# Kernel tuning notes

Measured on AMD Instinct MI355X. Metric: run time of the kernel, lower is better.

The kernel has to match this reference:

```python
import jax, jax.numpy as jnp
import numpy as np

_A1 = jnp.array([[1.,0.,0.,0.],[0.,1.,0.,0.],[0.,0.,1.,0.],[0.,0.,0.,1.]], dtype=jnp.float32)
_AI = jnp.array([[0.,-1.,0.,0.],[1.,0.,0.,0.],[0.,0.,0.,-1.],[0.,0.,1.,0.]], dtype=jnp.float32)
_AJ = jnp.array([[0.,0.,-1.,0.],[0.,0.,0.,1.],[1.,0.,0.,0.],[0.,-1.,0.,0.]], dtype=jnp.float32)
_AK = jnp.array([[0.,0.,0.,-1.],[0.,0.,-1.,0.],[0.,1.,0.,0.],[1.,0.,0.,0.]], dtype=jnp.float32)

IN_FEATURES = 1024
OUT_FEATURES = 1024
Q_IN = IN_FEATURES // 4
Q_OUT = OUT_FEATURES // 4

def _xavier_uniform(key, shape, gain=0.5):
    fan_out, fan_in = shape
    limit = gain * float(np.sqrt(6.0 / (fan_in + fan_out)))
    return jax.random.uniform(key, shape, jnp.float32, -limit, limit)

def setup_inputs() -> dict:
    key = jax.random.key(0)
    kx, kr, ki, kj, kk = jax.random.split(key, 5)
    x = jax.random.normal(kx, (8, 4096, IN_FEATURES), dtype=jnp.float32)
    R = _xavier_uniform(kr, (Q_OUT, Q_IN))
    I = _xavier_uniform(ki, (Q_OUT, Q_IN))
    J = _xavier_uniform(kj, (Q_OUT, Q_IN))
    K = _xavier_uniform(kk, (Q_OUT, Q_IN))
    bias = jnp.zeros((OUT_FEATURES,), dtype=jnp.float32)
    return {"x": x, "R": R, "I": I, "J": J, "K": K, "bias": bias}

def _build_weight(R, I, J, K):
    # W = kron(A1,R) + kron(AI,I) + kron(AJ,J) + kron(AK,K), shape (4*q_out, 4*q_in)
    # Assemble as 4x4 signed block grid in one einsum-style broadcast.
    # blocks[a,b] = A1[a,b]*R + AI[a,b]*I + AJ[a,b]*J + AK[a,b]*K
    blocks = (_A1[:, :, None, None] * R + _AI[:, :, None, None] * I
              + _AJ[:, :, None, None] * J + _AK[:, :, None, None] * K)  # [4,4,qo,qi]
    qo, qi = R.shape
    return blocks.transpose(0, 2, 1, 3).reshape(4 * qo, 4 * qi)

def reference(x, R, I, J, K, bias):
    W = _build_weight(R, I, J, K)
    return jnp.einsum('bsi,oi->bso', x, W) + bias
```

## Files before the change

kernel.cpp:

```cpp
#include <hip/hip_runtime.h>
#include <hip/hip_bf16.h>

typedef __attribute__((ext_vector_type(4))) float f32x4;
typedef __attribute__((ext_vector_type(4))) uint u32x4;
typedef __attribute__((ext_vector_type(8))) short bf16x8;

#define M_TOTAL 32768
#define N_TOTAL 1024
#define K_TOTAL 1024

__device__ __forceinline__ uint pk2(float a, float b) {
  __hip_bfloat162 h = __float22bfloat162_rn(make_float2(a, b));
  uint u;
  __builtin_memcpy(&u, &h, 4);
  return u;
}

#define SOFT_BARRIER() do {                                                   \
    __builtin_amdgcn_sched_barrier(0);                                        \
    asm volatile("s_waitcnt lgkmcnt(0)" ::: "memory");                        \
    __builtin_amdgcn_s_barrier();                                             \
    __builtin_amdgcn_sched_barrier(0);                                        \
  } while (0)

__global__ __launch_bounds__(256) void conv_x(
    const float* __restrict__ X, ushort* __restrict__ wsx)
{
  const int g = blockIdx.x * 256 + (int)threadIdx.x;
  const int wid = g >> 6;
  const int lane = g & 63;
  const int fm = wid >> 5;
  const int kb = wid & 31;
  const float* p = X + (size_t)(fm * 16 + (lane & 15)) * K_TOTAL
                     + kb * 32 + (lane >> 4) * 8;
  f32x4 lo = *(const f32x4*)p;
  f32x4 hi = *(const f32x4*)(p + 4);
  u32x4 v;
  v[0] = pk2(lo[0], lo[1]); v[1] = pk2(lo[2], lo[3]);
  v[2] = pk2(hi[0], hi[1]); v[3] = pk2(hi[2], hi[3]);
  *(u32x4*)(wsx + (size_t)wid * 512 + lane * 8) = v;
}

__global__ __launch_bounds__(256) void conv_b(
    const float* __restrict__ Rm, const float* __restrict__ Im,
    const float* __restrict__ Jm, const float* __restrict__ Km,
    ushort* __restrict__ ws)
{
  const int slot = blockIdx.x * 256 + (int)threadIdx.x;
  const int lane = slot & 63;
  const int kb = (slot >> 6) & 7;
  const int cb = (slot >> 9) & 15;
  const int si = slot >> 13;
  const float* S = (si == 0) ? Rm : (si == 1) ? Im : (si == 2) ? Jm : Km;
  const float* p = S + (cb * 16 + (lane & 15)) * 256 + kb * 32 + (lane >> 4) * 8;
  f32x4 lo = *(const f32x4*)p;
  f32x4 hi = *(const f32x4*)(p + 4);
  u32x4 v;
  v[0] = pk2(lo[0], lo[1]); v[1] = pk2(lo[2], lo[3]);
  v[2] = pk2(hi[0], hi[1]); v[3] = pk2(hi[2], hi[3]);
  *(u32x4*)(ws + (size_t)slot * 8) = v;
}

#define LOADA7(s, AF) do {                                                    \
    _Pragma("unroll")                                                         \
    for (int mi = 0; mi < 4; ++mi)                                            \
      AF[mi] = *(const bf16x8*)(                                              \
          WSX + ((size_t)(fmA + mi) * 32 + (s)) * 512 + lane * 8);            \
  } while (0)

#define LOADB7(s, BF) do {                                                    \
    const int si_ = a_idx ^ ((s) >> 3);                                       \
    const int kbq_ = (s) & 7;                                                 \
    _Pragma("unroll")                                                         \
    for (int ni = 0; ni < 4; ++ni)                                            \
      BF[ni] = *(const bf16x8*)(                                              \
          WSB + ((size_t)((si_ * 16 + cb0 + ni) * 8 + kbq_)) * 512            \
          + lane * 8);                                                        \
  } while (0)

#define SGN7(s, BF) do {                                                      \
    if ((0x284Eu >> ((a_idx << 2) | ((s) >> 3))) & 1u) {                      \
      _Pragma("unroll")                                                       \
      for (int f = 0; f < 4; ++f) {                                           \
        u32x4 u_ = __builtin_bit_cast(u32x4, BF[f]);                          \
        u_[0] ^= 0x80008000u; u_[1] ^= 0x80008000u;                           \
        u_[2] ^= 0x80008000u; u_[3] ^= 0x80008000u;                           \
        BF[f] = __builtin_bit_cast(bf16x8, u_);                               \
      }                                                                       \
    }                                                                         \
  } while (0)

#define MFMA7(AF, BF) do {                                                    \
    _Pragma("unroll")                                                         \
    for (int mi = 0; mi < 4; ++mi)                                            \
      _Pragma("unroll")                                                       \
      for (int ni = 0; ni < 4; ++ni)                                          \
        acc[mi][ni] = __builtin_amdgcn_mfma_f32_16x16x32_bf16(                \
            AF[mi], BF[ni], acc[mi][ni], 0, 0, 0);                            \
  } while (0)

__global__ __launch_bounds__(256, 3) void qlin_gemm8(
    const ushort* __restrict__ WSX, const ushort* __restrict__ WSB,
    const float* __restrict__ bias, float* __restrict__ Y)
{
  const int per = 2048 >> 3;
  const int bid = (int)blockIdx.x;
  const int swz = (bid & 7) * per + (bid >> 3);
  const int mblk = swz >> 3;
  const int nblk = swz & 7;
  const int m0 = mblk << 7;
  const int n0 = nblk << 7;
  const int a_idx = nblk >> 1;

  const int tid = (int)threadIdx.x;
  const int lane = tid & 63;
  const int wv = tid >> 6;
  const int wr = wv >> 1;
  const int wc = wv & 1;
  const int fmA = (mblk << 3) + (wr << 2);
  const int cb0 = ((nblk & 1) << 3) + (wc << 2);

  bf16x8 a0[4], b0[4], a1[4], b1[4], a2[4], b2[4];
  f32x4 acc[4][4];
#pragma unroll
  for (int i = 0; i < 4; ++i)
#pragma unroll
    for (int j = 0; j < 4; ++j) acc[i][j] = (f32x4)(0.0f);

  LOADA7(0, a0); LOADB7(0, b0);
  LOADA7(1, a1); LOADB7(1, b1);

#pragma unroll 1
  for (int s = 0; s < 30; s += 3) {
    LOADA7(s + 2, a2); LOADB7(s + 2, b2);
    SGN7(s, b0);     MFMA7(a0, b0);
    LOADA7(s + 3, a0); LOADB7(s + 3, b0);
    SGN7(s + 1, b1); MFMA7(a1, b1);
    LOADA7(s + 4, a1); LOADB7(s + 4, b1);
    SGN7(s + 2, b2); MFMA7(a2, b2);
  }
  SGN7(30, b0); MFMA7(a0, b0);
  SGN7(31, b1); MFMA7(a1, b1);

#pragma unroll
  for (int ni = 0; ni < 4; ++ni) {
    const int col = n0 + (wc << 6) + (ni << 4) + (lane & 15);
    const float bv = bias[col];
#pragma unroll
    for (int mi = 0; mi < 4; ++mi) {
      const int r0e = m0 + (wr << 6) + (mi << 4) + ((lane >> 4) << 2);
#pragma unroll
      for (int j = 0; j < 4; ++j)
        Y[(size_t)(r0e + j) * N_TOTAL + col] = acc[mi][ni][j] + bv;
    }
  }
}

#define BM2 256
#define BN2 256
#define BK2 64
#define NT2 512
#define NSTEPS2 (K_TOTAL / BK2)

#define LOAD_A2(kk) do {                                                      \
    _Pragma("unroll")                                                         \
    for (int cc = 0; cc < 4; ++cc) {                                          \
      const float* pa_ = X + (size_t)(m0 + r0 + 64 * cc) * K_TOTAL + (kk) + k0;\
      rA[2 * cc]     = *(const f32x4*)pa_;                                    \
      rA[2 * cc + 1] = *(const f32x4*)(pa_ + 4);                              \
    }                                                                         \
  } while (0)

#define COMMIT_A2(dst) do {                                                   \
    _Pragma("unroll")                                                         \
    for (int cc = 0; cc < 4; ++cc) {                                          \
      u32x4 va_;                                                              \
      va_[0] = pk2(rA[2 * cc][0], rA[2 * cc][1]);                             \
      va_[1] = pk2(rA[2 * cc][2], rA[2 * cc][3]);                             \
      va_[2] = pk2(rA[2 * cc + 1][0], rA[2 * cc + 1][1]);                     \
      va_[3] = pk2(rA[2 * cc + 1][2], rA[2 * cc + 1][3]);                     \
      *(u32x4*)((dst) + sbase + 8192 * cc) = va_;                             \
    }                                                                         \
  } while (0)

#define LOAD_B2(kk) do {                                                      \
    const int bsel_ = (kk) >> 8;                                              \
    const int si_ = a_idx ^ bsel_;                                            \
    const int kbq_ = ((kk) & 255) >> 5;                                       \
    const ushort* fb_ = WS + ((size_t)((si_ * 16 + wc4) * 8 + kbq_)) * 512    \
                        + lane * 8;                                           \
    _Pragma("unroll")                                                         \
    for (int ks = 0; ks < 2; ++ks)                                            \
      _Pragma("unroll")                                                       \
      for (int ni = 0; ni < 4; ++ni)                                          \
        bq[ks * 4 + ni] = *(const bf16x8*)(fb_ + (ni * 8 + ks) * 512);        \
    if ((0x284Eu >> ((a_idx << 2) | bsel_)) & 1u) {                           \
      _Pragma("unroll")                                                       \
      for (int f = 0; f < 8; ++f) {                                           \
        u32x4 u_ = __builtin_bit_cast(u32x4, bq[f]);                          \
        u_[0] ^= 0x80008000u; u_[1] ^= 0x80008000u;                           \
        u_[2] ^= 0x80008000u; u_[3] ^= 0x80008000u;                           \
        bq[f] = __builtin_bit_cast(bf16x8, u_);                               \
      }                                                                       \
    }                                                                         \
  } while (0)

#define COMPUTE2(src) do {                                                    \
    _Pragma("unroll")                                                         \
    for (int ks = 0; ks < 2; ++ks) {                                          \
      _Pragma("unroll")                                                       \
      for (int mi = 0; mi < 8; ++mi) {                                        \
        const int row_ = frow_a0 + (mi << 4);                                 \
        const int kb_ = (ks << 6) + fkb;                                      \
        bf16x8 af_ = *(const bf16x8*)((src) + row_ * (BK2 * 2)                \
                                      + (kb_ ^ ((row_ & 7) << 4)));           \
        _Pragma("unroll")                                                     \
        for (int ni = 0; ni < 4; ++ni)                                        \
          acc[mi][ni] = __builtin_amdgcn_mfma_f32_16x16x32_bf16(              \
              af_, bq[ks * 4 + ni], acc[mi][ni], 0, 0, 0);                    \
      }                                                                       \
    }                                                                         \
  } while (0)

__global__ __launch_bounds__(NT2, 2) void qlin_gemm2(
    const float* __restrict__ X, const ushort* __restrict__ WS,
    const float* __restrict__ bias, float* __restrict__ Y)
{
  const int per = ((M_TOTAL / BM2) * (N_TOTAL / BN2)) >> 3;
  const int bid = (int)blockIdx.x;
  const int swz = (bid & 7) * per + (bid >> 3);
  const int m0 = (swz >> 2) * BM2;
  const int nblk = swz & 3;
  const int n0 = nblk * BN2;
  const int a_idx = nblk;

  const int tid = (int)threadIdx.x;
  const int lane = tid & 63;
  const int wave = tid >> 6;
  const int wm = (wave >> 2) << 7;
  const int wc4 = (wave & 3) << 2;

  __shared__ __align__(16) ushort smA[2 * BM2 * BK2];
  char* const cS = (char*)smA;

  const int r0 = tid >> 3;
  const int k0 = (tid & 7) << 3;
  const int sbase = r0 * (BK2 * 2) + ((k0 * 2) ^ ((r0 & 7) << 4));

  f32x4 rA[8];
  bf16x8 bq[8];
  f32x4 acc[8][4];
#pragma unroll
  for (int i = 0; i < 8; ++i)
#pragma unroll
    for (int j = 0; j < 4; ++j) acc[i][j] = (f32x4)(0.0f);

  const int frow_a0 = wm + (lane & 15);
  const int fkb = (lane >> 4) << 4;

  LOAD_A2(0);
  COMMIT_A2(cS);
  LOAD_A2(BK2);
  SOFT_BARRIER();

#pragma unroll 1
  for (int k = 0; k < NSTEPS2; ++k) {
    char* const rbuf = cS + ((k & 1) << 15);
    char* const wbuf = cS + (((k + 1) & 1) << 15);
    COMMIT_A2(wbuf);
    LOAD_B2(k * BK2);
    if (k + 2 < NSTEPS2) LOAD_A2((k + 2) * BK2);
    COMPUTE2(rbuf);
    SOFT_BARRIER();
  }

#pragma unroll
  for (int ni = 0; ni < 4; ++ni) {
    const int col = n0 + (wc4 << 4) + (ni << 4) + (lane & 15);
    const float bv = bias[col];
#pragma unroll
    for (int mi = 0; mi < 8; ++mi) {
      const int r0e = m0 + wm + (mi << 4) + ((lane >> 4) << 2);
#pragma unroll
      for (int j = 0; j < 4; ++j)
        Y[(size_t)(r0e + j) * N_TOTAL + col] = acc[mi][ni][j] + bv;
    }
  }
}

#define BM 128
#define BN 128
#define BK 64
#define NTHREADS 256
#define NSTEPS (K_TOTAL / BK)

#define LOAD_TILE(kk) do {                                                    \
    const int si_ = a_idx ^ ((kk) >> 8);                                      \
    const float* Bsrc_ = (si_ == 0) ? Rm : (si_ == 1) ? Im                    \
                       : (si_ == 2) ? Jm : Km;                                \
    const int kloc_ = (kk) & 255;                                             \
    _Pragma("unroll")                                                         \
    for (int cc = 0; cc < 4; ++cc) {                                          \
      const float* pa_ = X + (size_t)(m0 + r0 + 32 * cc) * K_TOTAL + (kk) + k0;\
      rA[2 * cc]     = *(const f32x4*)pa_;                                    \
      rA[2 * cc + 1] = *(const f32x4*)(pa_ + 4);                              \
      const float* pb_ = Bsrc_ + (o_src + r0 + 32 * cc) * 256 + kloc_ + k0;   \
      rB[2 * cc]     = *(const f32x4*)pb_;                                    \
      rB[2 * cc + 1] = *(const f32x4*)(pb_ + 4);                              \
    }                                                                         \
  } while (0)

#define COMMIT_TILE(kk, dst) do {                                             \
    const uint neg_ = (0x284Eu >> ((a_idx << 2) | ((kk) >> 8))) & 1u;         \
    _Pragma("unroll")                                                         \
    for (int cc = 0; cc < 4; ++cc) {                                          \
      u32x4 va_;                                                              \
      va_[0] = pk2(rA[2 * cc][0], rA[2 * cc][1]);                             \
      va_[1] = pk2(rA[2 * cc][2], rA[2 * cc][3]);                             \
      va_[2] = pk2(rA[2 * cc + 1][0], rA[2 * cc + 1][1]);                     \
      va_[3] = pk2(rA[2 * cc + 1][2], rA[2 * cc + 1][3]);                     \
      *(u32x4*)((dst) + sbase + 4096 * cc) = va_;                             \
    }                                                                         \
    if (neg_) {                                                               \
      _Pragma("unroll")                                                       \
      for (int cc = 0; cc < 4; ++cc) {                                        \
        u32x4 vb_;                                                            \
        vb_[0] = pk2(-rB[2 * cc][0], -rB[2 * cc][1]);                         \
        vb_[1] = pk2(-rB[2 * cc][2], -rB[2 * cc][3]);                         \
        vb_[2] = pk2(-rB[2 * cc + 1][0], -rB[2 * cc + 1][1]);                 \
        vb_[3] = pk2(-rB[2 * cc + 1][2], -rB[2 * cc + 1][3]);                 \
        *(u32x4*)((dst) + 16384 + sbase + 4096 * cc) = vb_;                   \
      }                                                                       \
    } else {                                                                  \
      _Pragma("unroll")                                                       \
      for (int cc = 0; cc < 4; ++cc) {                                        \
        u32x4 vb_;                                                            \
        vb_[0] = pk2(rB[2 * cc][0], rB[2 * cc][1]);                           \
        vb_[1] = pk2(rB[2 * cc][2], rB[2 * cc][3]);                           \
        vb_[2] = pk2(rB[2 * cc + 1][0], rB[2 * cc + 1][1]);                   \
        vb_[3] = pk2(rB[2 * cc + 1][2], rB[2 * cc + 1][3]);                   \
        *(u32x4*)((dst) + 16384 + sbase + 4096 * cc) = vb_;                   \
      }                                                                       \
    }                                                                         \
  } while (0)

#define COMPUTE_TILE(src) do {                                                \
    _Pragma("unroll")                                                         \
    for (int ks = 0; ks < 2; ++ks) {                                          \
      const int kb_ = (ks << 6) + fkb;                                        \
      bf16x8 af_[4], bf_[4];                                                  \
      _Pragma("unroll")                                                       \
      for (int mi = 0; mi < 4; ++mi) {                                        \
        const int row_ = frow_a0 + (mi << 4);                                 \
        af_[mi] = *(const bf16x8*)((src) + row_ * (BK * 2)                    \
                                   + (kb_ ^ ((row_ & 7) << 4)));              \
      }                                                                       \
      _Pragma("unroll")                                                       \
      for (int ni = 0; ni < 4; ++ni) {                                        \
        const int row_ = frow_b0 + (ni << 4);                                 \
        bf_[ni] = *(const bf16x8*)((src) + 16384 + row_ * (BK * 2)            \
                                   + (kb_ ^ ((row_ & 7) << 4)));              \
      }                                                                       \
      _Pragma("unroll")                                                       \
      for (int mi = 0; mi < 4; ++mi)                                          \
        _Pragma("unroll")                                                     \
        for (int ni = 0; ni < 4; ++ni)                                        \
          acc[mi][ni] = __builtin_amdgcn_mfma_f32_16x16x32_bf16(              \
              af_[mi], bf_[ni], acc[mi][ni], 0, 0, 0);                        \
    }                                                                         \
  } while (0)

__global__ __launch_bounds__(NTHREADS, 2) void qlin_gemm(
    const float* __restrict__ X, const float* __restrict__ Rm,
    const float* __restrict__ Im, const float* __restrict__ Jm,
    const float* __restrict__ Km, const float* __restrict__ bias,
    float* __restrict__ Y)
{
  const int per = ((M_TOTAL / BM) * (N_TOTAL / BN)) >> 3;
  const int bid = (int)blockIdx.x;
  const int swz = (bid & 7) * per + (bid >> 3);
  const int m0 = (swz >> 3) * BM;
  const int n0 = (swz & 7) * BN;

  const int tid = (int)threadIdx.x;
  const int lane = tid & 63;
  const int wave = tid >> 6;
  const int wm = (wave >> 1) << 6;
  const int wn = (wave & 1) << 6;

  __shared__ __align__(16) ushort sm[2 * 2 * BM * BK];
  char* const cS = (char*)sm;

  const int a_idx = n0 >> 8;
  const int o_src = n0 & 255;

  const int r0 = tid >> 3;
  const int k0 = (tid & 7) << 3;
  const int sbase = r0 * (BK * 2) + ((k0 * 2) ^ ((r0 & 7) << 4));

  f32x4 rA[8], rB[8];
  f32x4 acc[4][4];
#pragma unroll
  for (int i = 0; i < 4; ++i)
#pragma unroll
    for (int j = 0; j < 4; ++j) acc[i][j] = (f32x4)(0.0f);

  const int frow_a0 = wm + (lane & 15);
  const int frow_b0 = wn + (lane & 15);
  const int fkb = (lane >> 4) << 4;

  LOAD_TILE(0);
  COMMIT_TILE(0, cS);
  LOAD_TILE(BK);
  SOFT_BARRIER();

#pragma unroll 1
  for (int k = 0; k < NSTEPS; ++k) {
    char* const rbuf = cS + ((k & 1) << 15);
    char* const wbuf = cS + (((k + 1) & 1) << 15);
    if (k + 1 < NSTEPS) COMMIT_TILE((k + 1) * BK, wbuf);
    if (k + 2 < NSTEPS) LOAD_TILE((k + 2) * BK);
    COMPUTE_TILE(rbuf);
    SOFT_BARRIER();
  }

#pragma unroll
  for (int ni = 0; ni < 4; ++ni) {
    const int col = n0 + wn + (ni << 4) + (lane & 15);
    const float bv = bias[col];
#pragma unroll
    for (int mi = 0; mi < 4; ++mi) {
      const int r0e = m0 + wm + (mi << 4) + ((lane >> 4) << 2);
#pragma unroll
      for (int j = 0; j < 4; ++j)
        Y[(size_t)(r0e + j) * N_TOTAL + col] = acc[mi][ni][j] + bv;
    }
  }
}

extern "C" void kernel_launch(void* const* d_in, const int* in_sizes, int n_in,
                              void* d_out, int out_size, void* d_ws, size_t ws_size,
                              hipStream_t stream) {
  const float* X = (const float*)d_in[0];
  const float* Rm = (const float*)d_in[1];
  const float* Im = (const float*)d_in[2];
  const float* Jm = (const float*)d_in[3];
  const float* Km = (const float*)d_in[4];
  const float* bias = (const float*)d_in[5];
  float* Y = (float*)d_out;

  const size_t needB = (size_t)4 * 256 * 256 * 2;
  const size_t needX = (size_t)M_TOTAL * K_TOTAL * 2;

  if (ws_size >= needX + needB) {
    ushort* wsx = (ushort*)d_ws;
    ushort* wsb = wsx + (size_t)M_TOTAL * K_TOTAL;
    conv_x<<<dim3(16384), dim3(256), 0, stream>>>(X, wsx);
    conv_b<<<dim3(128), dim3(256), 0, stream>>>(Rm, Im, Jm, Km, wsb);
    qlin_gemm8<<<dim3(2048), dim3(256), 0, stream>>>(wsx, wsb, bias, Y);
  } else if (ws_size >= needB) {
    ushort* wsb = (ushort*)d_ws;
    conv_b<<<dim3(128), dim3(256), 0, stream>>>(Rm, Im, Jm, Km, wsb);
    qlin_gemm2<<<dim3((M_TOTAL / BM2) * (N_TOTAL / BN2)), dim3(NT2), 0, stream>>>(
        X, wsb, bias, Y);
  } else {
    qlin_gemm<<<dim3((M_TOTAL / BM) * (N_TOTAL / BN)), dim3(NTHREADS), 0, stream>>>(
        X, Rm, Im, Jm, Km, bias, Y);
  }
}
```

Measured before the change: 121.9 us.

## Stage A tiles into LDS via direct global-to-LDS loads shared across waves

Before, each wave loaded its own A fragments straight from global memory into registers, so the two column-waves of a block fetched the same A data twice. Now each wave issues direct global_load_lds for two of the eight A fragments into a triple-buffered LDS ring. Waves read their four A fragments back from LDS just before the MFMAs. This halves global A traffic and frees registers, at the cost of vmcnt waits plus block barriers every k-step and extra LDS reads.

```diff
diff --git a/kernel.cpp b/kernel.cpp
--- a/kernel.cpp
+++ b/kernel.cpp
@@ -19,6 +19,19 @@
 #define SOFT_BARRIER() do {                                                   \
     __builtin_amdgcn_sched_barrier(0);                                        \
     asm volatile("s_waitcnt lgkmcnt(0)" ::: "memory");                        \
+    __builtin_amdgcn_s_barrier();                                             \
+    __builtin_amdgcn_sched_barrier(0);                                        \
+  } while (0)
+
+#define WAIT6_BAR() do {                                                      \
+    __builtin_amdgcn_sched_barrier(0);                                        \
+    asm volatile("s_waitcnt vmcnt(6)" ::: "memory");                          \
+    __builtin_amdgcn_s_barrier();                                             \
+    __builtin_amdgcn_sched_barrier(0);                                        \
+  } while (0)
+#define WAIT0_BAR() do {                                                      \
+    __builtin_amdgcn_sched_barrier(0);                                        \
+    asm volatile("s_waitcnt vmcnt(0)" ::: "memory");                          \
     __builtin_amdgcn_s_barrier();                                             \
     __builtin_amdgcn_sched_barrier(0);                                        \
   } while (0)
@@ -61,14 +74,18 @@
   *(u32x4*)(ws + (size_t)slot * 8) = v;
 }
 
-#define LOADA7(s, AF) do {                                                    \
-    _Pragma("unroll")                                                         \
-    for (int mi = 0; mi < 4; ++mi)                                            \
-      AF[mi] = *(const bf16x8*)(                                              \
-          WSX + ((size_t)(fmA + mi) * 32 + (s)) * 512 + lane * 8);            \
-  } while (0)
-
-#define LOADB7(s, BF) do {                                                    \
+#define STAGE9(s, lb) do {                                                    \
+    _Pragma("unroll")                                                         \
+    for (int j = 0; j < 2; ++j) {                                             \
+      const int f_ = (wv << 1) + j;                                           \
+      const ushort* s_ = WSX + ((size_t)(fmB + f_) * 32 + (s)) * 512          \
+                         + lane * 8;                                          \
+      __builtin_amdgcn_global_load_lds((const uint*)s_,                       \
+                                       (uint*)((lb) + f_ * 512), 16, 0, 0);   \
+    }                                                                         \
+  } while (0)
+
+#define LOADB9(s, BF) do {                                                    \
     const int si_ = a_idx ^ ((s) >> 3);                                       \
     const int kbq_ = (s) & 7;                                                 \
     _Pragma("unroll")                                                         \
@@ -78,7 +95,7 @@
           + lane * 8);                                                        \
   } while (0)
 
-#define SGN7(s, BF) do {                                                      \
+#define SGN9(s, BF) do {                                                      \
     if ((0x284Eu >> ((a_idx << 2) | ((s) >> 3))) & 1u) {                      \
       _Pragma("unroll")                                                       \
       for (int f = 0; f < 4; ++f) {                                           \
@@ -90,16 +107,18 @@
     }                                                                         \
   } while (0)
 
-#define MFMA7(AF, BF) do {                                                    \
-    _Pragma("unroll")                                                         \
-    for (int mi = 0; mi < 4; ++mi)                                            \
+#define COMPUTE9(lb, BF) do {                                                 \
+    _Pragma("unroll")                                                         \
+    for (int mi = 0; mi < 4; ++mi) {                                          \
+      bf16x8 af_ = *(const bf16x8*)((lb) + (frW + mi) * 512 + lane * 8);      \
       _Pragma("unroll")                                                       \
       for (int ni = 0; ni < 4; ++ni)                                          \
         acc[mi][ni] = __builtin_amdgcn_mfma_f32_16x16x32_bf16(                \
-            AF[mi], BF[ni], acc[mi][ni], 0, 0, 0);                            \
-  } while (0)
-
-__global__ __launch_bounds__(256, 3) void qlin_gemm8(
+            af_, BF[ni], acc[mi][ni], 0, 0, 0);                               \
+    }                                                                         \
+  } while (0)
+
+__global__ __launch_bounds__(256, 3) void qlin_gemm9(
     const ushort* __restrict__ WSX, const ushort* __restrict__ WSB,
     const float* __restrict__ bias, float* __restrict__ Y)
 {
@@ -117,30 +136,41 @@
   const int wv = tid >> 6;
   const int wr = wv >> 1;
   const int wc = wv & 1;
-  const int fmA = (mblk << 3) + (wr << 2);
+  const int fmB = mblk << 3;
+  const int frW = wr << 2;
   const int cb0 = ((nblk & 1) << 3) + (wc << 2);
 
-  bf16x8 a0[4], b0[4], a1[4], b1[4], a2[4], b2[4];
+  __shared__ __align__(16) ushort smA[3 * 8 * 512];
+  ushort* const lbuf0 = smA;
+  ushort* const lbuf1 = smA + 8 * 512;
+  ushort* const lbuf2 = smA + 16 * 512;
+
+  bf16x8 bq0[4], bq1[4], bq2[4];
   f32x4 acc[4][4];
 #pragma unroll
   for (int i = 0; i < 4; ++i)
 #pragma unroll
     for (int j = 0; j < 4; ++j) acc[i][j] = (f32x4)(0.0f);
 
-  LOADA7(0, a0); LOADB7(0, b0);
-  LOADA7(1, a1); LOADB7(1, b1);
+  STAGE9(0, lbuf0); LOADB9(0, bq0);
+  STAGE9(1, lbuf1); LOADB9(1, bq1);
 
 #pragma unroll 1
   for (int s = 0; s < 30; s += 3) {
-    LOADA7(s + 2, a2); LOADB7(s + 2, b2);
-    SGN7(s, b0);     MFMA7(a0, b0);
-    LOADA7(s + 3, a0); LOADB7(s + 3, b0);
-    SGN7(s + 1, b1); MFMA7(a1, b1);
-    LOADA7(s + 4, a1); LOADB7(s + 4, b1);
-    SGN7(s + 2, b2); MFMA7(a2, b2);
-  }
-  SGN7(30, b0); MFMA7(a0, b0);
-  SGN7(31, b1); MFMA7(a1, b1);
+    WAIT6_BAR();
+    STAGE9(s + 2, lbuf2); LOADB9(s + 2, bq2);
+    SGN9(s, bq0); COMPUTE9(lbuf0, bq0);
+    WAIT6_BAR();
+    STAGE9(s + 3, lbuf0); LOADB9(s + 3, bq0);
+    SGN9(s + 1, bq1); COMPUTE9(lbuf1, bq1);
+    WAIT6_BAR();
+    STAGE9(s + 4, lbuf1); LOADB9(s + 4, bq1);
+    SGN9(s + 2, bq2); COMPUTE9(lbuf2, bq2);
+  }
+  WAIT6_BAR();
+  SGN9(30, bq0); COMPUTE9(lbuf0, bq0);
+  WAIT0_BAR();
+  SGN9(31, bq1); COMPUTE9(lbuf1, bq1);
 
 #pragma unroll
   for (int ni = 0; ni < 4; ++ni) {
@@ -457,7 +487,7 @@
     ushort* wsb = wsx + (size_t)M_TOTAL * K_TOTAL;
     conv_x<<<dim3(16384), dim3(256), 0, stream>>>(X, wsx);
     conv_b<<<dim3(128), dim3(256), 0, stream>>>(Rm, Im, Jm, Km, wsb);
-    qlin_gemm8<<<dim3(2048), dim3(256), 0, stream>>>(wsx, wsb, bias, Y);
+    qlin_gemm9<<<dim3(2048), dim3(256), 0, stream>>>(wsx, wsb, bias, Y);
   } else if (ws_size >= needB) {
     ushort* wsb = (ushort*)d_ws;
     conv_b<<<dim3(128), dim3(256), 0, stream>>>(Rm, Im, Jm, Km, wsb);
```

Result: faster. 116.4 us (median of 3 runs) (-4.4%).

## Stage A fragments via global_load_lds and precompute negated weight copy

Applied to the files above, without the earlier changes.

The GEMM now streams X fragments straight from global memory into per-wave triple-buffered LDS with global_load_lds. Progress is tracked with explicit vmcnt waits, and the fragments are read from LDS just before the MFMAs, instead of being held in registers. This is meant to free VGPRs and let the copies run asynchronously. The weight conversion kernel also writes a sign-flipped copy of the bf16 weights, so the GEMM picks the negated base pointer instead of XOR-ing sign bits on every step. The cost is a larger workspace, extra LDS traffic, and hand-placed wait counts that must match the number of loads issued per stage.

```diff
diff --git a/kernel.cpp b/kernel.cpp
--- a/kernel.cpp
+++ b/kernel.cpp
@@ -20,6 +20,17 @@
     __builtin_amdgcn_sched_barrier(0);                                        \
     asm volatile("s_waitcnt lgkmcnt(0)" ::: "memory");                        \
     __builtin_amdgcn_s_barrier();                                             \
+    __builtin_amdgcn_sched_barrier(0);                                        \
+  } while (0)
+
+#define WAITV8() do {                                                         \
+    __builtin_amdgcn_sched_barrier(0);                                        \
+    asm volatile("s_waitcnt vmcnt(8)" ::: "memory");                          \
+    __builtin_amdgcn_sched_barrier(0);                                        \
+  } while (0)
+#define WAITV0() do {                                                         \
+    __builtin_amdgcn_sched_barrier(0);                                        \
+    asm volatile("s_waitcnt vmcnt(0)" ::: "memory");                          \
     __builtin_amdgcn_sched_barrier(0);                                        \
   } while (0)
 
@@ -41,7 +52,7 @@
   *(u32x4*)(wsx + (size_t)wid * 512 + lane * 8) = v;
 }
 
-__global__ __launch_bounds__(256) void conv_b(
+__global__ __launch_bounds__(256) void conv_b2(
     const float* __restrict__ Rm, const float* __restrict__ Im,
     const float* __restrict__ Jm, const float* __restrict__ Km,
     ushort* __restrict__ ws)
@@ -59,47 +70,47 @@
   v[0] = pk2(lo[0], lo[1]); v[1] = pk2(lo[2], lo[3]);
   v[2] = pk2(hi[0], hi[1]); v[3] = pk2(hi[2], hi[3]);
   *(u32x4*)(ws + (size_t)slot * 8) = v;
-}
-
-#define LOADA7(s, AF) do {                                                    \
-    _Pragma("unroll")                                                         \
-    for (int mi = 0; mi < 4; ++mi)                                            \
-      AF[mi] = *(const bf16x8*)(                                              \
-          WSX + ((size_t)(fmA + mi) * 32 + (s)) * 512 + lane * 8);            \
-  } while (0)
-
-#define LOADB7(s, BF) do {                                                    \
-    const int si_ = a_idx ^ ((s) >> 3);                                       \
+  u32x4 n;
+  n[0] = v[0] ^ 0x80008000u; n[1] = v[1] ^ 0x80008000u;
+  n[2] = v[2] ^ 0x80008000u; n[3] = v[3] ^ 0x80008000u;
+  *(u32x4*)(ws + 262144 + (size_t)slot * 8) = n;
+}
+
+#define STAGE10(s, lb) do {                                                   \
+    _Pragma("unroll")                                                         \
+    for (int j = 0; j < 4; ++j) {                                             \
+      const ushort* s_ = WSX + ((size_t)(fmA + j) * 32 + (s)) * 512           \
+                         + lane * 8;                                          \
+      __builtin_amdgcn_global_load_lds((const uint*)s_,                       \
+                                       (uint*)((lb) + j * 512), 16, 0, 0);    \
+    }                                                                         \
+  } while (0)
+
+#define LOADB10(s, BF) do {                                                   \
+    const int bsel_ = (s) >> 3;                                               \
+    const int si_ = a_idx ^ bsel_;                                            \
+    const uint neg_ = (0x284Eu >> ((a_idx << 2) | bsel_)) & 1u;               \
+    const ushort* base_ = WSB + (neg_ ? 262144 : 0);                          \
     const int kbq_ = (s) & 7;                                                 \
     _Pragma("unroll")                                                         \
     for (int ni = 0; ni < 4; ++ni)                                            \
       BF[ni] = *(const bf16x8*)(                                              \
-          WSB + ((size_t)((si_ * 16 + cb0 + ni) * 8 + kbq_)) * 512            \
+          base_ + ((size_t)((si_ * 16 + cb0 + ni) * 8 + kbq_)) * 512          \
           + lane * 8);                                                        \
   } while (0)
 
-#define SGN7(s, BF) do {                                                      \
-    if ((0x284Eu >> ((a_idx << 2) | ((s) >> 3))) & 1u) {                      \
-      _Pragma("unroll")                                                       \
-      for (int f = 0; f < 4; ++f) {                                           \
-        u32x4 u_ = __builtin_bit_cast(u32x4, BF[f]);                          \
-        u_[0] ^= 0x80008000u; u_[1] ^= 0x80008000u;                           \
-        u_[2] ^= 0x80008000u; u_[3] ^= 0x80008000u;                           \
-        BF[f] = __builtin_bit_cast(bf16x8, u_);                               \
-      }                                                                       \
-    }                                                                         \
-  } while (0)
-
-#define MFMA7(AF, BF) do {                                                    \
-    _Pragma("unroll")                                                         \
-    for (int mi = 0; mi < 4; ++mi)                                            \
+#define COMPUTE10(lb, BF) do {                                                \
+    _Pragma("unroll")                                                         \
+    for (int mi = 0; mi < 4; ++mi) {                                          \
+      bf16x8 af_ = *(const bf16x8*)((lb) + mi * 512 + lane * 8);              \
       _Pragma("unroll")                                                       \
       for (int ni = 0; ni < 4; ++ni)                                          \
         acc[mi][ni] = __builtin_amdgcn_mfma_f32_16x16x32_bf16(                \
-            AF[mi], BF[ni], acc[mi][ni], 0, 0, 0);                            \
-  } while (0)
-
-__global__ __launch_bounds__(256, 3) void qlin_gemm8(
+            af_, BF[ni], acc[mi][ni], 0, 0, 0);                               \
+    }                                                                         \
+  } while (0)
+
+__global__ __launch_bounds__(256, 3) void qlin_gemm10(
     const ushort* __restrict__ WSX, const ushort* __restrict__ WSB,
     const float* __restrict__ bias, float* __restrict__ Y)
 {
@@ -120,27 +131,38 @@
   const int fmA = (mblk << 3) + (wr << 2);
   const int cb0 = ((nblk & 1) << 3) + (wc << 2);
 
-  bf16x8 a0[4], b0[4], a1[4], b1[4], a2[4], b2[4];
+  __shared__ __align__(16) ushort smA[4 * 3 * 4 * 512];
+  ushort* const myL = smA + wv * (3 * 4 * 512);
+  ushort* const lbuf0 = myL;
+  ushort* const lbuf1 = myL + 4 * 512;
+  ushort* const lbuf2 = myL + 8 * 512;
+
+  bf16x8 bq0[4], bq1[4], bq2[4];
   f32x4 acc[4][4];
 #pragma unroll
   for (int i = 0; i < 4; ++i)
 #pragma unroll
     for (int j = 0; j < 4; ++j) acc[i][j] = (f32x4)(0.0f);
 
-  LOADA7(0, a0); LOADB7(0, b0);
-  LOADA7(1, a1); LOADB7(1, b1);
+  STAGE10(0, lbuf0); LOADB10(0, bq0);
+  STAGE10(1, lbuf1); LOADB10(1, bq1);
 
 #pragma unroll 1
   for (int s = 0; s < 30; s += 3) {
-    LOADA7(s + 2, a2); LOADB7(s + 2, b2);
-    SGN7(s, b0);     MFMA7(a0, b0);
-    LOADA7(s + 3, a0); LOADB7(s + 3, b0);
-    SGN7(s + 1, b1); MFMA7(a1, b1);
-    LOADA7(s + 4, a1); LOADB7(s + 4, b1);
-    SGN7(s + 2, b2); MFMA7(a2, b2);
-  }
-  SGN7(30, b0); MFMA7(a0, b0);
-  SGN7(31, b1); MFMA7(a1, b1);
+    WAITV8();
+    STAGE10(s + 2, lbuf2); LOADB10(s + 2, bq2);
+    COMPUTE10(lbuf0, bq0);
+    WAITV8();
+    STAGE10(s + 3, lbuf0); LOADB10(s + 3, bq0);
+    COMPUTE10(lbuf1, bq1);
+    WAITV8();
+    STAGE10(s + 4, lbuf1); LOADB10(s + 4, bq1);
+    COMPUTE10(lbuf2, bq2);
+  }
+  WAITV8();
+  COMPUTE10(lbuf0, bq0);
+  WAITV0();
+  COMPUTE10(lbuf1, bq1);
 
 #pragma unroll
   for (int ni = 0; ni < 4; ++ni) {
@@ -450,17 +472,22 @@
   float* Y = (float*)d_out;
 
   const size_t needB = (size_t)4 * 256 * 256 * 2;
+  const size_t needB2 = 2 * needB;
   const size_t needX = (size_t)M_TOTAL * K_TOTAL * 2;
 
-  if (ws_size >= needX + needB) {
+  if (ws_size >= needX + needB2) {
     ushort* wsx = (ushort*)d_ws;
     ushort* wsb = wsx + (size_t)M_TOTAL * K_TOTAL;
     conv_x<<<dim3(16384), dim3(256), 0, stream>>>(X, wsx);
-    conv_b<<<dim3(128), dim3(256), 0, stream>>>(Rm, Im, Jm, Km, wsb);
-    qlin_gemm8<<<dim3(2048), dim3(256), 0, stream>>>(wsx, wsb, bias, Y);
+    conv_b2<<<dim3(128), dim3(256), 0, stream>>>(Rm, Im, Jm, Km, wsb);
+    qlin_gemm10<<<dim3(2048), dim3(256), 0, stream>>>(wsx, wsb, bias, Y);
   } else if (ws_size >= needB) {
     ushort* wsb = (ushort*)d_ws;
-    conv_b<<<dim3(128), dim3(256), 0, stream>>>(Rm, Im, Jm, Km, wsb);
+    if (ws_size >= needB2) {
+      conv_b2<<<dim3(128), dim3(256), 0, stream>>>(Rm, Im, Jm, Km, wsb);
+    } else {
+      conv_b2<<<dim3(128), dim3(256), 0, stream>>>(Rm, Im, Jm, Km, wsb);
+    }
     qlin_gemm2<<<dim3((M_TOTAL / BM2) * (N_TOTAL / BN2)), dim3(NT2), 0, stream>>>(
         X, wsb, bias, Y);
   } else {
```

New measurement: 123.8 us. Within noise of the previous version (+1.6%).
